# Kernel tuning notes

Hardware: AMD Instinct MI355X
Metric: run time of the kernel (lower is better)

The kernel has to match this reference:

```python
import math
import jax, jax.numpy as jnp
import numpy as np

B, T, D, V, L, H = 2, 1024, 768, 32768, 4, 12
HD = D // H
STD = 0.02


def layer_norm(x, w, b):
    mu = x.mean(-1, keepdims=True)
    var = ((x - mu) ** 2).mean(-1, keepdims=True)
    return (x - mu) * jax.lax.rsqrt(var + 1e-5) * w + b


def new_gelu(x):
    c = math.sqrt(2.0 / math.pi)
    return 0.5 * x * (1.0 + jnp.tanh(c * (x + 0.044715 * x ** 3)))


def setup_inputs() -> dict:
    key = jax.random.key(0)
    ks = jax.random.split(key, 10)
    idx = jax.random.randint(ks[0], (B, T), 0, V)
    age = jax.random.uniform(ks[1], (B, T), dtype=jnp.float32) * 36500.0  # days
    wte = jax.random.normal(ks[2], (V, D), jnp.float32) * STD  # tied with lm_head
    wae_w = jax.random.normal(ks[3], (D, D), jnp.float32) * STD  # AgeEncoding linear (no bias)
    proj_std = STD / math.sqrt(2 * L)
    return {
        'idx': idx,
        'age': age,
        'wte': wte,
        'wae_w': wae_w,
        'ln1_w': jnp.ones((L, D), jnp.float32),
        'ln1_b': jnp.zeros((L, D), jnp.float32),
        'attn_w': jax.random.normal(ks[4], (L, 3 * D, D), jnp.float32) * STD,
        'attn_b': jnp.zeros((L, 3 * D), jnp.float32),
        'proj_w': jax.random.normal(ks[5], (L, D, D), jnp.float32) * proj_std,
        'proj_b': jnp.zeros((L, D), jnp.float32),
        'ln2_w': jnp.ones((L, D), jnp.float32),
        'ln2_b': jnp.zeros((L, D), jnp.float32),
        'fc_w': jax.random.normal(ks[6], (L, 4 * D, D), jnp.float32) * STD,
        'fc_b': jnp.zeros((L, 4 * D), jnp.float32),
        'fc2_w': jax.random.normal(ks[7], (L, D, 4 * D), jnp.float32) * proj_std,
        'fc2_b': jnp.zeros((L, D), jnp.float32),
        'lnf_w': jnp.ones((D,), jnp.float32),
        'lnf_b': jnp.zeros((D,), jnp.float32),
    }


def _forward(idx, age, wte, wae_w, ln1_w, ln1_b, attn_w, attn_b, proj_w, proj_b,
             ln2_w, ln2_b, fc_w, fc_b, fc2_w, fc2_b, lnf_w, lnf_b):
    # token embedding (tied with lm_head)
    tok = wte[idx]  # [B,T,D]
    # age encoding: interleaved sin/cos of age/365.25 * div_term, then linear
    div = jnp.exp(jnp.arange(0, D, 2).astype(jnp.float32) * (-math.log(10000.0) / D))  # [D/2]
    ang = (age[..., None] / 365.25) * div  # [B,T,D/2]
    y = jnp.zeros((B, T, D), tok.dtype)
    y = y.at[..., 0::2].set(jnp.sin(ang)).at[..., 1::2].set(jnp.cos(ang))
    x = tok + y @ wae_w.T  # token_drop identity at dropout 0 (scaled by 1-0)

    # attention mask: valid-token outer product, causal, plus self-attn for pad tokens
    valid = idx > 0
    tril = jnp.tril(jnp.ones((T, T), bool))
    mask = valid[:, None, None, :] & valid[:, None, :, None] & tril
    mask = (mask | ((~valid)[:, None, None, :] & jnp.eye(T, dtype=bool))) & tril  # [B,1,T,T]

    scale = 1.0 / math.sqrt(HD)

    def block(x, p):
        l1w, l1b, aw, ab, pw, pb, l2w, l2b, fw, fb, f2w, f2b = p
        h = layer_norm(x, l1w, l1b)
        qkv = h @ aw.T + ab
        q, k, v = jnp.split(qkv, 3, axis=-1)
        q = q.reshape(B, T, H, HD).transpose(0, 2, 1, 3)  # [B,H,T,HD]
        k = k.reshape(B, T, H, HD).transpose(0, 2, 1, 3)
        v = v.reshape(B, T, H, HD).transpose(0, 2, 1, 3)
        att = jnp.einsum('bhqd,bhkd->bhqk', q, k) * scale
        att = jnp.where(mask, att, -jnp.inf)
        att = jax.nn.softmax(att, axis=-1)
        yv = jnp.einsum('bhqk,bhkd->bhqd', att, v)
        yv = yv.transpose(0, 2, 1, 3).reshape(B, T, D)
        x = x + yv @ pw.T + pb
        h2 = layer_norm(x, l2w, l2b)
        x = x + new_gelu(h2 @ fw.T + fb) @ f2w.T + f2b
        return x, att

    x, att = jax.lax.scan(block, x, (ln1_w, ln1_b, attn_w, attn_b, proj_w, proj_b,
                                     ln2_w, ln2_b, fc_w, fc_b, fc2_w, fc2_b))
    x = layer_norm(x, lnf_w, lnf_b)
    logits = x @ wte.T  # tied lm_head
    return logits


def reference(idx, age, wte, wae_w, ln1_w, ln1_b, attn_w, attn_b, proj_w, proj_b,
              ln2_w, ln2_b, fc_w, fc_b, fc2_w, fc2_b, lnf_w, lnf_b):
    return _forward(idx, age, wte, wae_w, ln1_w, ln1_b, attn_w, attn_b, proj_w, proj_b,
                    ln2_w, ln2_b, fc_w, fc_b, fc2_w, fc2_b, lnf_w, lnf_b)
```

## Files before the change

### kernel.cpp

```cpp
#include <hip/hip_runtime.h>

typedef unsigned short u16;
typedef __bf16 bf16x8 __attribute__((ext_vector_type(8)));
typedef float f32x4 __attribute__((ext_vector_type(4)));

__device__ __forceinline__ u16 f2bf(float f) {
    union { float f; unsigned int u; } c; c.f = f;
    unsigned int u = c.u;
    unsigned int r = (u + 0x7FFFu + ((u >> 16) & 1u)) >> 16;
    return (u16)r;
}

__device__ __forceinline__ float gelu_f(float v) {
    const float c = 0.7978845608028654f;
    float t = tanhf(c * (v + 0.044715f * v * v * v));
    return 0.5f * v * (1.0f + t);
}

typedef const __attribute__((address_space(1))) unsigned int* as1_u32p;
typedef __attribute__((address_space(3))) unsigned int* as3_u32p;
typedef const __attribute__((address_space(3))) u16* as3_cu16p;
__device__ __forceinline__ void gload16(const void* g, void* l) {
    __builtin_amdgcn_global_load_lds((as1_u32p)g, (as3_u32p)l, 16, 0, 0);
}

__device__ __forceinline__ bf16x8 ds_read_frag(const u16* p) {
    bf16x8 r;
    as3_cu16p lp = (as3_cu16p)p;
    asm volatile("ds_read_b128 %0, %1" : "=v"(r) : "v"(lp));
    return r;
}

template <int N> __device__ __forceinline__ void wait_vmcnt() {
    if constexpr (N == 0)      asm volatile("s_waitcnt vmcnt(0)" ::: "memory");
    else if constexpr (N == 3) asm volatile("s_waitcnt vmcnt(3)" ::: "memory");
    else if constexpr (N == 4) asm volatile("s_waitcnt vmcnt(4)" ::: "memory");
    else if constexpr (N == 6) asm volatile("s_waitcnt vmcnt(6)" ::: "memory");
    else if constexpr (N == 8) asm volatile("s_waitcnt vmcnt(8)" ::: "memory");
}

__global__ __launch_bounds__(256) void cvt_kernel(
    const float* __restrict__ src, u16* __restrict__ dst, int n4)
{
    int i = blockIdx.x * 256 + threadIdx.x;
    int stride = gridDim.x * 256;
    for (; i < n4; i += stride) {
        float4 f = reinterpret_cast<const float4*>(src)[i];
        union { u16 h[4]; uint2 u; } cv;
        cv.h[0] = f2bf(f.x); cv.h[1] = f2bf(f.y);
        cv.h[2] = f2bf(f.z); cv.h[3] = f2bf(f.w);
        reinterpret_cast<uint2*>(dst)[i] = cv.u;
    }
}

__global__ __launch_bounds__(256) void embed_kernel(
    const int* __restrict__ idx, const float* __restrict__ age,
    const float* __restrict__ wte, float* __restrict__ x, u16* __restrict__ y)
{
    int t = blockIdx.x;
    int tid = threadIdx.x;
    int tok = idx[t];
    float a = age[t] * (1.0f / 365.25f);
    const float kc = -9.210340371976184f / 768.0f;
#pragma unroll
    for (int j = 0; j < 3; j++) {
        int d = tid + j * 256;
        x[(size_t)t * 768 + d] = wte[(size_t)tok * 768 + d];
        int twoi = d & ~1;
        float dv = __expf(kc * (float)twoi);
        float ang = a * dv;
        float val = (d & 1) ? __cosf(ang) : __sinf(ang);
        y[(size_t)t * 768 + d] = f2bf(val);
    }
}

__global__ __launch_bounds__(256) void ln_kernel(
    const float* __restrict__ x, const float* __restrict__ w,
    const float* __restrict__ b, u16* __restrict__ out)
{
    int row = blockIdx.x;
    int tid = threadIdx.x;
    int l = tid & 63, wv = tid >> 6;
    const float* xr = x + (size_t)row * 768;
    float v[3], s = 0.f, ss = 0.f;
#pragma unroll
    for (int j = 0; j < 3; j++) { v[j] = xr[tid + j * 256]; s += v[j]; ss += v[j] * v[j]; }
#pragma unroll
    for (int d = 1; d < 64; d <<= 1) { s += __shfl_xor(s, d); ss += __shfl_xor(ss, d); }
    __shared__ float ps[4], pss[4];
    if (l == 0) { ps[wv] = s; pss[wv] = ss; }
    __syncthreads();
    s = ps[0] + ps[1] + ps[2] + ps[3];
    ss = pss[0] + pss[1] + pss[2] + pss[3];
    float mu = s * (1.0f / 768.0f);
    float var = ss * (1.0f / 768.0f) - mu * mu;
    float rstd = rsqrtf(var + 1e-5f);
#pragma unroll
    for (int j = 0; j < 3; j++) {
        int d = tid + j * 256;
        out[(size_t)row * 768 + d] = f2bf((v[j] - mu) * rstd * w[d] + b[d]);
    }
}

enum { EPI_BF16 = 0, EPI_BF16_GELU = 1, EPI_F32_RESID = 2, EPI_F32 = 3 };

template <int EPI, int BM, int NWM>
__global__ __launch_bounds__(256) void gemm_p2_kernel(
    const u16* __restrict__ A, const u16* __restrict__ B,
    const float* __restrict__ bias, const float* resid, void* out,
    int N, int K, int mtiles, int nwg8)
{
    constexpr int NWN = 4 / NWM;
    constexpr int MI  = (BM / NWM) / 16;
    constexpr int NI  = (128 / NWN) / 16;
    constexpr int ASHOTS = (BM * 4) / 256;
    constexpr int LPS = ASHOTS + 2;
    __shared__ u16 As[3][BM][32];
    __shared__ u16 Bs[3][128][32];
    int tid = threadIdx.x;
    int l = tid & 63, w = tid >> 6;
    int lw = l & 15, lg = l >> 4;
    int bid = blockIdx.x;
    int wg = (bid & 7) * nwg8 + (bid >> 3);
    int mt = wg % mtiles, nt = wg / mtiles;
    int row0 = mt * BM, col0 = nt * 128;
    int wm = w % NWM, wn = w / NWM;
    int mbase = wm * (BM / NWM), nbase = wn * (128 / NWN);

    const u16* ga = A + (size_t)(row0 + (tid >> 2)) * K + (tid & 3) * 8;
    const u16* gb = B + (size_t)(col0 + (tid >> 2)) * K + (tid & 3) * 8;
    const size_t k64 = (size_t)64 * K;
    int dofs = tid * 8;

    f32x4 acc[MI][NI] = {};
    const int ntiles = K >> 5;

    auto stage = [&](int nb, int kk) {
        u16* asb = &As[nb][0][0];
        u16* bsb = &Bs[nb][0][0];
#pragma unroll
        for (int s = 0; s < ASHOTS; s++)
            gload16(ga + s * k64 + kk, asb + s * 2048 + dofs);
#pragma unroll
        for (int s = 0; s < 2; s++)
            gload16(gb + s * k64 + kk, bsb + s * 2048 + dofs);
    };

    stage(0, 0);
    stage(1, 32);
    wait_vmcnt<LPS>();
    __builtin_amdgcn_s_barrier();

    int cur = 0;
    for (int t = 0; t < ntiles; ++t) {
        int prv = cur == 0 ? 2 : cur - 1;
        if (t + 2 < ntiles) stage(prv, (t + 2) << 5);
        bf16x8 af[MI], bfr[NI];
#pragma unroll
        for (int mi = 0; mi < MI; mi++)
            af[mi] = ds_read_frag(&As[cur][mbase + mi * 16 + lw][lg * 8]);
#pragma unroll
        for (int ni = 0; ni < NI; ni++)
            bfr[ni] = ds_read_frag(&Bs[cur][nbase + ni * 16 + lw][lg * 8]);
        asm volatile("s_waitcnt lgkmcnt(0)" ::: "memory");
        __builtin_amdgcn_sched_barrier(0);
        __builtin_amdgcn_s_setprio(1);
#pragma unroll
        for (int mi = 0; mi < MI; mi++)
#pragma unroll
            for (int ni = 0; ni < NI; ni++)
                acc[mi][ni] = __builtin_amdgcn_mfma_f32_16x16x32_bf16(af[mi], bfr[ni], acc[mi][ni], 0, 0, 0);
        __builtin_amdgcn_s_setprio(0);
        if (t + 2 < ntiles)      wait_vmcnt<LPS>();
        else if (t + 1 < ntiles) wait_vmcnt<0>();
        __builtin_amdgcn_s_barrier();
        cur = cur == 2 ? 0 : cur + 1;
    }

#pragma unroll
    for (int mi = 0; mi < MI; mi++) {
#pragma unroll
        for (int ni = 0; ni < NI; ni++) {
            int colc = col0 + nbase + ni * 16 + lw;
            float bv = bias ? bias[colc] : 0.0f;
#pragma unroll
            for (int j = 0; j < 4; j++) {
                int row = row0 + mbase + mi * 16 + lg * 4 + j;
                size_t off = (size_t)row * N + colc;
                float v = acc[mi][ni][j] + bv;
                if constexpr (EPI == EPI_BF16) {
                    ((u16*)out)[off] = f2bf(v);
                } else if constexpr (EPI == EPI_BF16_GELU) {
                    ((u16*)out)[off] = f2bf(gelu_f(v));
                } else if constexpr (EPI == EPI_F32_RESID) {
                    ((float*)out)[off] = v + resid[off];
                } else {
                    ((float*)out)[off] = v;
                }
            }
        }
    }
}

template <int EPI>
__global__ __launch_bounds__(256) void gemm_kernel(
    const u16* __restrict__ A, const float* __restrict__ Bw,
    const float* __restrict__ bias, const float* resid, void* out,
    int N, int K)
{
    constexpr int M = 2048;
    __shared__ u16 As[128][40];
    __shared__ u16 Bs[128][40];
    int tid = threadIdx.x;
    int l = tid & 63, w = tid >> 6;
    int lw = l & 15, lg = l >> 4;
    int mtiles = M / 128;
    int mt = blockIdx.x % mtiles, nt = blockIdx.x / mtiles;
    int row0 = mt * 128, col0 = nt * 128;
    int mbase = (w & 1) * 64, nbase = (w >> 1) * 64;
    f32x4 acc[4][4] = {};

    for (int kk = 0; kk < K; kk += 32) {
        int c = tid;
#pragma unroll
        for (int i = 0; i < 2; i++, c += 256) {
            int r = c >> 2, q = c & 3;
            uint4 u = *reinterpret_cast<const uint4*>(A + (size_t)(row0 + r) * K + kk + q * 8);
            *reinterpret_cast<uint4*>(&As[r][q * 8]) = u;
        }
        int c2 = tid;
#pragma unroll
        for (int i = 0; i < 4; i++, c2 += 256) {
            int r = c2 >> 3, q = c2 & 7;
            const float4 f = *reinterpret_cast<const float4*>(Bw + (size_t)(col0 + r) * K + kk + q * 4);
            union { u16 h[4]; uint2 u; } cv;
            cv.h[0] = f2bf(f.x); cv.h[1] = f2bf(f.y); cv.h[2] = f2bf(f.z); cv.h[3] = f2bf(f.w);
            *reinterpret_cast<uint2*>(&Bs[r][q * 4]) = cv.u;
        }
        __syncthreads();
        bf16x8 af[4], bfr[4];
#pragma unroll
        for (int mi = 0; mi < 4; mi++)
            af[mi] = *reinterpret_cast<const bf16x8*>(&As[mbase + mi * 16 + lw][lg * 8]);
#pragma unroll
        for (int ni = 0; ni < 4; ni++)
            bfr[ni] = *reinterpret_cast<const bf16x8*>(&Bs[nbase + ni * 16 + lw][lg * 8]);
#pragma unroll
        for (int mi = 0; mi < 4; mi++)
#pragma unroll
            for (int ni = 0; ni < 4; ni++)
                acc[mi][ni] = __builtin_amdgcn_mfma_f32_16x16x32_bf16(af[mi], bfr[ni], acc[mi][ni], 0, 0, 0);
        __syncthreads();
    }

#pragma unroll
    for (int mi = 0; mi < 4; mi++) {
#pragma unroll
        for (int ni = 0; ni < 4; ni++) {
            int colc = col0 + nbase + ni * 16 + lw;
            float bv = bias ? bias[colc] : 0.0f;
#pragma unroll
            for (int j = 0; j < 4; j++) {
                int row = row0 + mbase + mi * 16 + lg * 4 + j;
                size_t off = (size_t)row * N + colc;
                float v = acc[mi][ni][j] + bv;
                if constexpr (EPI == EPI_BF16) {
                    ((u16*)out)[off] = f2bf(v);
                } else if constexpr (EPI == EPI_BF16_GELU) {
                    ((u16*)out)[off] = f2bf(gelu_f(v));
                } else if constexpr (EPI == EPI_F32_RESID) {
                    ((float*)out)[off] = v + resid[off];
                } else {
                    ((float*)out)[off] = v;
                }
            }
        }
    }
}

__global__ __launch_bounds__(256) void attn_kernel(
    const u16* __restrict__ qkv, const int* __restrict__ idx, u16* __restrict__ yv)
{
    __shared__ u16 Kt[32][72];
    __shared__ u16 Vt[64][40];
    __shared__ u16 Pb[4][16][40];
    __shared__ int kval[32];

    int tid = threadIdx.x, l = tid & 63, w = tid >> 6;
    int lw = l & 15, lg = l >> 4;
    int bid = blockIdx.x;
    int qb = bid & 15;
    int h = (bid >> 4) % 12;
    int b = bid / (16 * 12);
    const size_t base = (size_t)b * 1024;

    int qrow = qb * 64 + w * 16 + lw;
    const u16* qp = qkv + (base + qrow) * 2304 + h * 64;
    bf16x8 aq0 = *reinterpret_cast<const bf16x8*>(qp + lg * 8);
    bf16x8 aq1 = *reinterpret_cast<const bf16x8*>(qp + 32 + lg * 8);

    int rowj[4], vq[4];
#pragma unroll
    for (int j = 0; j < 4; j++) {
        rowj[j] = qb * 64 + w * 16 + lg * 4 + j;
        vq[j] = idx[base + rowj[j]] > 0;
    }
    float m[4], lsum[4];
    f32x4 O[4] = {};
#pragma unroll
    for (int j = 0; j < 4; j++) { m[j] = -__builtin_inff(); lsum[j] = 0.0f; }

    int kvend = qb * 64 + 64;
    for (int kv0 = 0; kv0 < kvend; kv0 += 32) {
        {
            int r = tid >> 3, cc = tid & 7;
            const u16* kp = qkv + (base + kv0 + r) * 2304 + 768 + h * 64 + cc * 8;
            uint4 ku = *reinterpret_cast<const uint4*>(kp);
            *reinterpret_cast<uint4*>(&Kt[r][cc * 8]) = ku;
            const u16* vp = qkv + (base + kv0 + r) * 2304 + 1536 + h * 64 + cc * 8;
            union { uint4 u; u16 h8[8]; } vu;
            vu.u = *reinterpret_cast<const uint4*>(vp);
#pragma unroll
            for (int j2 = 0; j2 < 8; j2++) Vt[cc * 8 + j2][r] = vu.h8[j2];
            if (tid < 32) kval[tid] = idx[base + kv0 + tid] > 0;
        }
        __syncthreads();

        f32x4 S[2];
#pragma unroll
        for (int g = 0; g < 2; g++) {
            bf16x8 bk0 = *reinterpret_cast<const bf16x8*>(&Kt[g * 16 + lw][lg * 8]);
            bf16x8 bk1 = *reinterpret_cast<const bf16x8*>(&Kt[g * 16 + lw][32 + lg * 8]);
            f32x4 t = {};
            t = __builtin_amdgcn_mfma_f32_16x16x32_bf16(aq0, bk0, t, 0, 0, 0);
            t = __builtin_amdgcn_mfma_f32_16x16x32_bf16(aq1, bk1, t, 0, 0, 0);
            S[g] = t;
        }
        float p[2][4];
#pragma unroll
        for (int j = 0; j < 4; j++) {
            float sv0, sv1;
#pragma unroll
            for (int g = 0; g < 2; g++) {
                int kcol = kv0 + g * 16 + lw;
                float s = S[g][j] * 0.125f;
                bool keep = (kcol <= rowj[j]) &&
                            ((vq[j] && kval[g * 16 + lw]) || (kcol == rowj[j]));
                s = keep ? s : -__builtin_inff();
                if (g) sv1 = s; else sv0 = s;
            }
            float mx = fmaxf(sv0, sv1);
            mx = fmaxf(mx, __shfl_xor(mx, 1));
            mx = fmaxf(mx, __shfl_xor(mx, 2));
            mx = fmaxf(mx, __shfl_xor(mx, 4));
            mx = fmaxf(mx, __shfl_xor(mx, 8));
            float mn = fmaxf(m[j], mx);
            float mclamp = fmaxf(mn, -1e30f);
            float scale = __expf(m[j] - mclamp);
            float p0 = __expf(sv0 - mclamp);
            float p1 = __expf(sv1 - mclamp);
            float rs = p0 + p1;
            rs += __shfl_xor(rs, 1); rs += __shfl_xor(rs, 2);
            rs += __shfl_xor(rs, 4); rs += __shfl_xor(rs, 8);
            lsum[j] = lsum[j] * scale + rs;
            m[j] = mn;
#pragma unroll
            for (int ni = 0; ni < 4; ni++) O[ni][j] *= scale;
            p[0][j] = p0; p[1][j] = p1;
        }
#pragma unroll
        for (int g = 0; g < 2; g++)
#pragma unroll
            for (int j = 0; j < 4; j++)
                Pb[w][lg * 4 + j][g * 16 + lw] = f2bf(p[g][j]);
        bf16x8 ap = *reinterpret_cast<const bf16x8*>(&Pb[w][lw][lg * 8]);
#pragma unroll
        for (int ni = 0; ni < 4; ni++) {
            bf16x8 bv = *reinterpret_cast<const bf16x8*>(&Vt[ni * 16 + lw][lg * 8]);
            O[ni] = __builtin_amdgcn_mfma_f32_16x16x32_bf16(ap, bv, O[ni], 0, 0, 0);
        }
        __syncthreads();
    }

#pragma unroll
    for (int j = 0; j < 4; j++) {
        float inv = 1.0f / lsum[j];
#pragma unroll
        for (int ni = 0; ni < 4; ni++) {
            float v = O[ni][j] * inv;
            yv[(base + rowj[j]) * 768 + h * 64 + ni * 16 + lw] = f2bf(v);
        }
    }
}

static void launch_gemm_db(int epi, const u16* A, const u16* B, const float* bias,
                           const float* resid, void* out, int N, int K, hipStream_t s)
{
    dim3 blk(256);
    if (N == 768) {
        constexpr int BM = 64, NWM = 1;
        int mtiles = 2048 / BM;
        int nwg = mtiles * (N / 128);
        dim3 grid(nwg);
        int nwg8 = nwg / 8;
        switch (epi) {
            case EPI_BF16:      gemm_p2_kernel<EPI_BF16, BM, NWM><<<grid, blk, 0, s>>>(A, B, bias, resid, out, N, K, mtiles, nwg8); break;
            case EPI_BF16_GELU: gemm_p2_kernel<EPI_BF16_GELU, BM, NWM><<<grid, blk, 0, s>>>(A, B, bias, resid, out, N, K, mtiles, nwg8); break;
            case EPI_F32_RESID: gemm_p2_kernel<EPI_F32_RESID, BM, NWM><<<grid, blk, 0, s>>>(A, B, bias, resid, out, N, K, mtiles, nwg8); break;
            default:            gemm_p2_kernel<EPI_F32, BM, NWM><<<grid, blk, 0, s>>>(A, B, bias, resid, out, N, K, mtiles, nwg8); break;
        }
    } else {
        constexpr int BM = 128, NWM = 2;
        int mtiles = 2048 / BM;
        int nwg = mtiles * (N / 128);
        dim3 grid(nwg);
        int nwg8 = nwg / 8;
        switch (epi) {
            case EPI_BF16:      gemm_p2_kernel<EPI_BF16, BM, NWM><<<grid, blk, 0, s>>>(A, B, bias, resid, out, N, K, mtiles, nwg8); break;
            case EPI_BF16_GELU: gemm_p2_kernel<EPI_BF16_GELU, BM, NWM><<<grid, blk, 0, s>>>(A, B, bias, resid, out, N, K, mtiles, nwg8); break;
            case EPI_F32_RESID: gemm_p2_kernel<EPI_F32_RESID, BM, NWM><<<grid, blk, 0, s>>>(A, B, bias, resid, out, N, K, mtiles, nwg8); break;
            default:            gemm_p2_kernel<EPI_F32, BM, NWM><<<grid, blk, 0, s>>>(A, B, bias, resid, out, N, K, mtiles, nwg8); break;
        }
    }
}

static void launch_gemm_f32w(int epi, const u16* A, const float* Bw, const float* bias,
                             const float* resid, void* out, int N, int K, hipStream_t s)
{
    dim3 grid((2048 / 128) * (N / 128)), blk(256);
    switch (epi) {
        case EPI_BF16:      gemm_kernel<EPI_BF16><<<grid, blk, 0, s>>>(A, Bw, bias, resid, out, N, K); break;
        case EPI_BF16_GELU: gemm_kernel<EPI_BF16_GELU><<<grid, blk, 0, s>>>(A, Bw, bias, resid, out, N, K); break;
        case EPI_F32_RESID: gemm_kernel<EPI_F32_RESID><<<grid, blk, 0, s>>>(A, Bw, bias, resid, out, N, K); break;
        default:            gemm_kernel<EPI_F32><<<grid, blk, 0, s>>>(A, Bw, bias, resid, out, N, K); break;
    }
}

static void cvt(const float* src, u16* dst, size_t n, hipStream_t s) {
    int n4 = (int)(n / 4);
    int blocks = (n4 + 255) / 256;
    if (blocks > 2048) blocks = 2048;
    cvt_kernel<<<blocks, 256, 0, s>>>(src, dst, n4);
}

extern "C" void kernel_launch(void* const* d_in, const int* in_sizes, int n_in,
                              void* d_out, int out_size, void* d_ws, size_t ws_size,
                              hipStream_t stream)
{
    (void)in_sizes; (void)n_in; (void)out_size;
    const int*   idx    = (const int*)  d_in[0];
    const float* age    = (const float*)d_in[1];
    const float* wte    = (const float*)d_in[2];
    const float* wae_w  = (const float*)d_in[3];
    const float* ln1_w  = (const float*)d_in[4];
    const float* ln1_b  = (const float*)d_in[5];
    const float* attn_w = (const float*)d_in[6];
    const float* attn_b = (const float*)d_in[7];
    const float* proj_w = (const float*)d_in[8];
    const float* proj_b = (const float*)d_in[9];
    const float* ln2_w  = (const float*)d_in[10];
    const float* ln2_b  = (const float*)d_in[11];
    const float* fc_w   = (const float*)d_in[12];
    const float* fc_b   = (const float*)d_in[13];
    const float* fc2_w  = (const float*)d_in[14];
    const float* fc2_b  = (const float*)d_in[15];
    const float* lnf_w  = (const float*)d_in[16];
    const float* lnf_b  = (const float*)d_in[17];

    char* ws = (char*)d_ws;
    size_t off = 0;
    float* x   = (float*)(ws + off); off += (size_t)2048 * 768 * 4;
    u16* hb    = (u16*)(ws + off);   off += (size_t)2048 * 768 * 2;
    u16* qkvb  = (u16*)(ws + off);   off += (size_t)2048 * 2304 * 2;
    u16* yvb   = (u16*)(ws + off);   off += (size_t)2048 * 768 * 2;
    u16* a1b   = (u16*)(ws + off);   off += (size_t)2048 * 3072 * 2;
    u16* yage  = (u16*)(ws + off);   off += (size_t)2048 * 768 * 2;
    u16* wte_b  = (u16*)(ws + off);  off += (size_t)32768 * 768 * 2;
    u16* attn_wb= (u16*)(ws + off);  off += (size_t)4 * 2304 * 768 * 2;
    u16* proj_wb= (u16*)(ws + off);  off += (size_t)4 * 768 * 768 * 2;
    u16* fc_wb  = (u16*)(ws + off);  off += (size_t)4 * 3072 * 768 * 2;
    u16* fc2_wb = (u16*)(ws + off);  off += (size_t)4 * 768 * 3072 * 2;
    u16* wae_wb = (u16*)(ws + off);  off += (size_t)768 * 768 * 2;
    const size_t NEED = off;

    if (ws_size >= NEED) {
        cvt(wte,    wte_b,   (size_t)32768 * 768, stream);
        cvt(attn_w, attn_wb, (size_t)4 * 2304 * 768, stream);
        cvt(proj_w, proj_wb, (size_t)4 * 768 * 768, stream);
        cvt(fc_w,   fc_wb,   (size_t)4 * 3072 * 768, stream);
        cvt(fc2_w,  fc2_wb,  (size_t)4 * 768 * 3072, stream);
        cvt(wae_w,  wae_wb,  (size_t)768 * 768, stream);

        embed_kernel<<<2048, 256, 0, stream>>>(idx, age, wte, x, yage);
        launch_gemm_db(EPI_F32_RESID, yage, wae_wb, nullptr, x, x, 768, 768, stream);

        for (int li = 0; li < 4; li++) {
            ln_kernel<<<2048, 256, 0, stream>>>(x, ln1_w + li * 768, ln1_b + li * 768, hb);
            launch_gemm_db(EPI_BF16, hb, attn_wb + (size_t)li * 2304 * 768, attn_b + li * 2304,
                           nullptr, qkvb, 2304, 768, stream);
            attn_kernel<<<2 * 12 * 16, 256, 0, stream>>>(qkvb, idx, yvb);
            launch_gemm_db(EPI_F32_RESID, yvb, proj_wb + (size_t)li * 768 * 768, proj_b + li * 768,
                           x, x, 768, 768, stream);
            ln_kernel<<<2048, 256, 0, stream>>>(x, ln2_w + li * 768, ln2_b + li * 768, hb);
            launch_gemm_db(EPI_BF16_GELU, hb, fc_wb + (size_t)li * 3072 * 768, fc_b + li * 3072,
                           nullptr, a1b, 3072, 768, stream);
            launch_gemm_db(EPI_F32_RESID, a1b, fc2_wb + (size_t)li * 768 * 3072, fc2_b + li * 768,
                           x, x, 768, 3072, stream);
        }

        ln_kernel<<<2048, 256, 0, stream>>>(x, lnf_w, lnf_b, hb);
        launch_gemm_db(EPI_F32, hb, wte_b, nullptr, nullptr, d_out, 32768, 768, stream);
    } else {
        embed_kernel<<<2048, 256, 0, stream>>>(idx, age, wte, x, yage);
        launch_gemm_f32w(EPI_F32_RESID, yage, wae_w, nullptr, x, x, 768, 768, stream);
        for (int li = 0; li < 4; li++) {
            ln_kernel<<<2048, 256, 0, stream>>>(x, ln1_w + li * 768, ln1_b + li * 768, hb);
            launch_gemm_f32w(EPI_BF16, hb, attn_w + (size_t)li * 2304 * 768, attn_b + li * 2304,
                             nullptr, qkvb, 2304, 768, stream);
            attn_kernel<<<2 * 12 * 16, 256, 0, stream>>>(qkvb, idx, yvb);
            launch_gemm_f32w(EPI_F32_RESID, yvb, proj_w + (size_t)li * 768 * 768, proj_b + li * 768,
                             x, x, 768, 768, stream);
            ln_kernel<<<2048, 256, 0, stream>>>(x, ln2_w + li * 768, ln2_b + li * 768, hb);
            launch_gemm_f32w(EPI_BF16_GELU, hb, fc_w + (size_t)li * 3072 * 768, fc_b + li * 3072,
                             nullptr, a1b, 3072, 768, stream);
            launch_gemm_f32w(EPI_F32_RESID, a1b, fc2_w + (size_t)li * 768 * 3072, fc2_b + li * 768,
                             x, x, 768, 3072, stream);
        }
        ln_kernel<<<2048, 256, 0, stream>>>(x, lnf_w, lnf_b, hb);
        launch_gemm_f32w(EPI_F32, hb, wte, nullptr, nullptr, d_out, 32768, 768, stream);
    }
}
```

Baseline: 1.476 ms.

## Use K=64 tiles with XOR-swizzled LDS layout in a single GEMM config

```diff
diff --git a/kernel.cpp b/kernel.cpp
--- a/kernel.cpp
+++ b/kernel.cpp
@@ -33,8 +33,6 @@
 
 template <int N> __device__ __forceinline__ void wait_vmcnt() {
     if constexpr (N == 0)      asm volatile("s_waitcnt vmcnt(0)" ::: "memory");
-    else if constexpr (N == 3) asm volatile("s_waitcnt vmcnt(3)" ::: "memory");
-    else if constexpr (N == 4) asm volatile("s_waitcnt vmcnt(4)" ::: "memory");
     else if constexpr (N == 6) asm volatile("s_waitcnt vmcnt(6)" ::: "memory");
     else if constexpr (N == 8) asm volatile("s_waitcnt vmcnt(8)" ::: "memory");
 }
@@ -104,88 +102,95 @@
 
 enum { EPI_BF16 = 0, EPI_BF16_GELU = 1, EPI_F32_RESID = 2, EPI_F32 = 3 };
 
-template <int EPI, int BM, int NWM>
-__global__ __launch_bounds__(256) void gemm_p2_kernel(
+template <int EPI>
+__global__ __launch_bounds__(256) void gemm_sw_kernel(
     const u16* __restrict__ A, const u16* __restrict__ B,
     const float* __restrict__ bias, const float* resid, void* out,
     int N, int K, int mtiles, int nwg8)
 {
-    constexpr int NWN = 4 / NWM;
-    constexpr int MI  = (BM / NWM) / 16;
-    constexpr int NI  = (128 / NWN) / 16;
-    constexpr int ASHOTS = (BM * 4) / 256;
-    constexpr int LPS = ASHOTS + 2;
-    __shared__ u16 As[3][BM][32];
-    __shared__ u16 Bs[3][128][32];
+    constexpr int LPS = 6;
+    __shared__ u16 As[3][64][64];
+    __shared__ u16 Bs[3][128][64];
     int tid = threadIdx.x;
     int l = tid & 63, w = tid >> 6;
     int lw = l & 15, lg = l >> 4;
+    int lw7 = lw & 7;
     int bid = blockIdx.x;
     int wg = (bid & 7) * nwg8 + (bid >> 3);
     int mt = wg % mtiles, nt = wg / mtiles;
-    int row0 = mt * BM, col0 = nt * 128;
-    int wm = w % NWM, wn = w / NWM;
-    int mbase = wm * (BM / NWM), nbase = wn * (128 / NWN);
-
-    const u16* ga = A + (size_t)(row0 + (tid >> 2)) * K + (tid & 3) * 8;
-    const u16* gb = B + (size_t)(col0 + (tid >> 2)) * K + (tid & 3) * 8;
-    const size_t k64 = (size_t)64 * K;
+    int row0 = mt * 64, col0 = nt * 128;
+    int nbase = w * 32;
+
+    int cq = (tid & 7) ^ ((tid >> 3) & 7);
+    const u16* gaw = A + (size_t)(row0 + (tid >> 3)) * K + cq * 8;
+    const u16* gbw = B + (size_t)(col0 + (tid >> 3)) * K + cq * 8;
+    const size_t k32 = (size_t)32 * K;
     int dofs = tid * 8;
 
-    f32x4 acc[MI][NI] = {};
-    const int ntiles = K >> 5;
+    f32x4 acc[4][2] = {};
+    const int ntiles = K >> 6;
 
     auto stage = [&](int nb, int kk) {
         u16* asb = &As[nb][0][0];
         u16* bsb = &Bs[nb][0][0];
 #pragma unroll
-        for (int s = 0; s < ASHOTS; s++)
-            gload16(ga + s * k64 + kk, asb + s * 2048 + dofs);
-#pragma unroll
         for (int s = 0; s < 2; s++)
-            gload16(gb + s * k64 + kk, bsb + s * 2048 + dofs);
+            gload16(gaw + s * k32 + kk, asb + s * 2048 + dofs);
+#pragma unroll
+        for (int s = 0; s < 4; s++)
+            gload16(gbw + s * k32 + kk, bsb + s * 2048 + dofs);
     };
 
     stage(0, 0);
-    stage(1, 32);
+    stage(1, 64);
     wait_vmcnt<LPS>();
     __builtin_amdgcn_s_barrier();
 
     int cur = 0;
     for (int t = 0; t < ntiles; ++t) {
-        int prv = cur == 0 ? 2 : cur - 1;
-        if (t + 2 < ntiles) stage(prv, (t + 2) << 5);
-        bf16x8 af[MI], bfr[NI];
-#pragma unroll
-        for (int mi = 0; mi < MI; mi++)
-            af[mi] = ds_read_frag(&As[cur][mbase + mi * 16 + lw][lg * 8]);
-#pragma unroll
-        for (int ni = 0; ni < NI; ni++)
-            bfr[ni] = ds_read_frag(&Bs[cur][nbase + ni * 16 + lw][lg * 8]);
+        int nxt = cur + 2 >= 3 ? cur - 1 : cur + 2;
+        if (t + 2 < ntiles) stage(nxt, (t + 2) << 6);
+        bf16x8 af[4][2], bf[2][2];
+#pragma unroll
+        for (int mi = 0; mi < 4; mi++)
+#pragma unroll
+            for (int kh = 0; kh < 2; kh++) {
+                int slot = (kh * 4 + lg) ^ lw7;
+                af[mi][kh] = ds_read_frag(&As[cur][mi * 16 + lw][slot * 8]);
+            }
+#pragma unroll
+        for (int ni = 0; ni < 2; ni++)
+#pragma unroll
+            for (int kh = 0; kh < 2; kh++) {
+                int slot = (kh * 4 + lg) ^ lw7;
+                bf[ni][kh] = ds_read_frag(&Bs[cur][nbase + ni * 16 + lw][slot * 8]);
+            }
         asm volatile("s_waitcnt lgkmcnt(0)" ::: "memory");
         __builtin_amdgcn_sched_barrier(0);
         __builtin_amdgcn_s_setprio(1);
 #pragma unroll
-        for (int mi = 0; mi < MI; mi++)
-#pragma unroll
-            for (int ni = 0; ni < NI; ni++)
-                acc[mi][ni] = __builtin_amdgcn_mfma_f32_16x16x32_bf16(af[mi], bfr[ni], acc[mi][ni], 0, 0, 0);
+        for (int kh = 0; kh < 2; kh++)
+#pragma unroll
+            for (int mi = 0; mi < 4; mi++)
+#pragma unroll
+                for (int ni = 0; ni < 2; ni++)
+                    acc[mi][ni] = __builtin_amdgcn_mfma_f32_16x16x32_bf16(af[mi][kh], bf[ni][kh], acc[mi][ni], 0, 0, 0);
         __builtin_amdgcn_s_setprio(0);
         if (t + 2 < ntiles)      wait_vmcnt<LPS>();
         else if (t + 1 < ntiles) wait_vmcnt<0>();
         __builtin_amdgcn_s_barrier();
-        cur = cur == 2 ? 0 : cur + 1;
-    }
-
-#pragma unroll
-    for (int mi = 0; mi < MI; mi++) {
-#pragma unroll
-        for (int ni = 0; ni < NI; ni++) {
+        cur = cur + 1 >= 3 ? 0 : cur + 1;
+    }
+
+#pragma unroll
+    for (int mi = 0; mi < 4; mi++) {
+#pragma unroll
+        for (int ni = 0; ni < 2; ni++) {
             int colc = col0 + nbase + ni * 16 + lw;
             float bv = bias ? bias[colc] : 0.0f;
 #pragma unroll
             for (int j = 0; j < 4; j++) {
-                int row = row0 + mbase + mi * 16 + lg * 4 + j;
+                int row = row0 + mi * 16 + lg * 4 + j;
                 size_t off = (size_t)row * N + colc;
                 float v = acc[mi][ni][j] + bv;
                 if constexpr (EPI == EPI_BF16) {
@@ -393,34 +398,18 @@
     }
 }
 
-static void launch_gemm_db(int epi, const u16* A, const u16* B, const float* bias,
+static void launch_gemm_sw(int epi, const u16* A, const u16* B, const float* bias,
                            const float* resid, void* out, int N, int K, hipStream_t s)
 {
-    dim3 blk(256);
-    if (N == 768) {
-        constexpr int BM = 64, NWM = 1;
-        int mtiles = 2048 / BM;
-        int nwg = mtiles * (N / 128);
-        dim3 grid(nwg);
-        int nwg8 = nwg / 8;
-        switch (epi) {
-            case EPI_BF16:      gemm_p2_kernel<EPI_BF16, BM, NWM><<<grid, blk, 0, s>>>(A, B, bias, resid, out, N, K, mtiles, nwg8); break;
-            case EPI_BF16_GELU: gemm_p2_kernel<EPI_BF16_GELU, BM, NWM><<<grid, blk, 0, s>>>(A, B, bias, resid, out, N, K, mtiles, nwg8); break;
-            case EPI_F32_RESID: gemm_p2_kernel<EPI_F32_RESID, BM, NWM><<<grid, blk, 0, s>>>(A, B, bias, resid, out, N, K, mtiles, nwg8); break;
-            default:            gemm_p2_kernel<EPI_F32, BM, NWM><<<grid, blk, 0, s>>>(A, B, bias, resid, out, N, K, mtiles, nwg8); break;
-        }
-    } else {
-        constexpr int BM = 128, NWM = 2;
-        int mtiles = 2048 / BM;
-        int nwg = mtiles * (N / 128);
-        dim3 grid(nwg);
-        int nwg8 = nwg / 8;
-        switch (epi) {
-            case EPI_BF16:      gemm_p2_kernel<EPI_BF16, BM, NWM><<<grid, blk, 0, s>>>(A, B, bias, resid, out, N, K, mtiles, nwg8); break;
-            case EPI_BF16_GELU: gemm_p2_kernel<EPI_BF16_GELU, BM, NWM><<<grid, blk, 0, s>>>(A, B, bias, resid, out, N, K, mtiles, nwg8); break;
-            case EPI_F32_RESID: gemm_p2_kernel<EPI_F32_RESID, BM, NWM><<<grid, blk, 0, s>>>(A, B, bias, resid, out, N, K, mtiles, nwg8); break;
-            default:            gemm_p2_kernel<EPI_F32, BM, NWM><<<grid, blk, 0, s>>>(A, B, bias, resid, out, N, K, mtiles, nwg8); break;
-        }
+    int mtiles = 2048 / 64;
+    int nwg = mtiles * (N / 128);
+    dim3 grid(nwg), blk(256);
+    int nwg8 = nwg / 8;
+    switch (epi) {
+        case EPI_BF16:      gemm_sw_kernel<EPI_BF16><<<grid, blk, 0, s>>>(A, B, bias, resid, out, N, K, mtiles, nwg8); break;
+        case EPI_BF16_GELU: gemm_sw_kernel<EPI_BF16_GELU><<<grid, blk, 0, s>>>(A, B, bias, resid, out, N, K, mtiles, nwg8); break;
+        case EPI_F32_RESID: gemm_sw_kernel<EPI_F32_RESID><<<grid, blk, 0, s>>>(A, B, bias, resid, out, N, K, mtiles, nwg8); break;
+        default:            gemm_sw_kernel<EPI_F32><<<grid, blk, 0, s>>>(A, B, bias, resid, out, N, K, mtiles, nwg8); break;
     }
 }
 
@@ -492,24 +481,24 @@
         cvt(wae_w,  wae_wb,  (size_t)768 * 768, stream);
 
         embed_kernel<<<2048, 256, 0, stream>>>(idx, age, wte, x, yage);
-        launch_gemm_db(EPI_F32_RESID, yage, wae_wb, nullptr, x, x, 768, 768, stream);
+        launch_gemm_sw(EPI_F32_RESID, yage, wae_wb, nullptr, x, x, 768, 768, stream);
 
         for (int li = 0; li < 4; li++) {
             ln_kernel<<<2048, 256, 0, stream>>>(x, ln1_w + li * 768, ln1_b + li * 768, hb);
-            launch_gemm_db(EPI_BF16, hb, attn_wb + (size_t)li * 2304 * 768, attn_b + li * 2304,
+            launch_gemm_sw(EPI_BF16, hb, attn_wb + (size_t)li * 2304 * 768, attn_b + li * 2304,
                            nullptr, qkvb, 2304, 768, stream);
             attn_kernel<<<2 * 12 * 16, 256, 0, stream>>>(qkvb, idx, yvb);
-            launch_gemm_db(EPI_F32_RESID, yvb, proj_wb + (size_t)li * 768 * 768, proj_b + li * 768,
+            launch_gemm_sw(EPI_F32_RESID, yvb, proj_wb + (size_t)li * 768 * 768, proj_b + li * 768,
                            x, x, 768, 768, stream);
             ln_kernel<<<2048, 256, 0, stream>>>(x, ln2_w + li * 768, ln2_b + li * 768, hb);
-            launch_gemm_db(EPI_BF16_GELU, hb, fc_wb + (size_t)li * 3072 * 768, fc_b + li * 3072,
+            launch_gemm_sw(EPI_BF16_GELU, hb, fc_wb + (size_t)li * 3072 * 768, fc_b + li * 3072,
                            nullptr, a1b, 3072, 768, stream);
-            launch_gemm_db(EPI_F32_RESID, a1b, fc2_wb + (size_t)li * 768 * 3072, fc2_b + li * 768,
+            launch_gemm_sw(EPI_F32_RESID, a1b, fc2_wb + (size_t)li * 768 * 3072, fc2_b + li * 768,
                            x, x, 768, 3072, stream);
         }
 
         ln_kernel<<<2048, 256, 0, stream>>>(x, lnf_w, lnf_b, hb);
-        launch_gemm_db(EPI_F32, hb, wte_b, nullptr, nullptr, d_out, 32768, 768, stream);
+        launch_gemm_sw(EPI_F32, hb, wte_b, nullptr, nullptr, d_out, 32768, 768, stream);
     } else {
         embed_kernel<<<2048, 256, 0, stream>>>(idx, age, wte, x, yage);
         launch_gemm_f32w(EPI_F32_RESID, yage, wae_w, nullptr, x, x, 768, 768, stream);
```

New measurement: 1.614 ms. 9.3% more time.
